# Kernel tuning notes

Hardware: AMD Instinct MI355X
Metric: run time of the kernel (lower is better)

Reference implementation:

```python
import jax, jax.numpy as jnp
import numpy as np

N_NODES = 50000
N_EDGES = 800000
N_PAIRS = 262144
F_IN, H1, H2, NCLS, HEADS = 572, 256, 128, 65, 2


def _bn(x, g, b, eps=1e-5):
    mu = x.mean(axis=0)
    var = x.var(axis=0)
    return g * (x - mu) * jax.lax.rsqrt(var + eps) + b


def _gat_conv(x, src, dst, W, a_src, a_dst, bias, heads, ch):
    """PyG GATConv, concat=False (mean over heads), negative_slope=0.2."""
    n = x.shape[0]
    h = (x @ W).reshape(n, heads, ch)                     # [N,H,C]
    s_n = (h * a_src[None]).sum(-1)                       # [N,H]
    d_n = (h * a_dst[None]).sum(-1)                       # [N,H]
    alpha = jax.nn.leaky_relu(s_n[src] + d_n[dst], 0.2)   # [E,H]
    m = jax.ops.segment_max(alpha, dst, num_segments=n)
    m = jnp.where(jnp.isfinite(m), m, 0.0)
    e = jnp.exp(alpha - m[dst])
    z = jax.ops.segment_sum(e, dst, num_segments=n)
    w = e / (z[dst] + 1e-16)                              # edge softmax per dst
    msg = h[src] * w[:, :, None]                          # [E,H,C]
    out = jax.ops.segment_sum(msg, dst, num_segments=n)   # [N,H,C]
    return out.mean(axis=1) + bias                        # concat=False -> mean


def setup_inputs() -> dict:
    key = jax.random.key(0)
    ks = jax.random.split(key, 24)
    g = lambda k, shp, fan: jax.random.normal(k, shp, jnp.float32) * (1.0 / np.sqrt(fan))
    inp = {
        "edge_index": jax.random.randint(ks[0], (2, N_EDGES), 0, N_NODES, jnp.int32),
        "x": jax.random.normal(ks[1], (N_NODES, F_IN), jnp.float32),
        "edge_id": jax.random.randint(ks[2], (2, N_PAIRS), 0, N_NODES, jnp.int32),
        "W1": g(ks[3], (F_IN, HEADS * H1), F_IN),
        "a_src1": g(ks[4], (HEADS, H1), H1),
        "a_dst1": g(ks[5], (HEADS, H1), H1),
        "b1": jnp.zeros((H1,), jnp.float32),
        "bn1_g": jnp.ones((H1,), jnp.float32), "bn1_b": jnp.zeros((H1,), jnp.float32),
        "W2": g(ks[6], (H1, HEADS * H1), H1),
        "a_src2": g(ks[7], (HEADS, H1), H1),
        "a_dst2": g(ks[8], (HEADS, H1), H1),
        "b2": jnp.zeros((H1,), jnp.float32),
        "bn2_g": jnp.ones((H1,), jnp.float32), "bn2_b": jnp.zeros((H1,), jnp.float32),
        "lw1": g(ks[9], (2 * H1, H2), 2 * H1), "lb1": jnp.zeros((H2,), jnp.float32),
        "bn3_g": jnp.ones((H2,), jnp.float32), "bn3_b": jnp.zeros((H2,), jnp.float32),
        "lw2": g(ks[10], (H2, H2), H2), "lb2": jnp.zeros((H2,), jnp.float32),
        "bn4_g": jnp.ones((H2,), jnp.float32), "bn4_b": jnp.zeros((H2,), jnp.float32),
        "fw": g(ks[11], (H2, NCLS), H2), "fb": jnp.zeros((NCLS,), jnp.float32),
    }
    return inp


def reference(edge_index, x, edge_id,
              W1, a_src1, a_dst1, b1, bn1_g, bn1_b,
              W2, a_src2, a_dst2, b2, bn2_g, bn2_b,
              lw1, lb1, bn3_g, bn3_b,
              lw2, lb2, bn4_g, bn4_b,
              fw, fb):
    n = x.shape[0]
    # PyG GATConv default add_self_loops=True
    loops = jnp.arange(n, dtype=edge_index.dtype)
    src = jnp.concatenate([edge_index[0], loops])
    dst = jnp.concatenate([edge_index[1], loops])

    h = _gat_conv(x, src, dst, W1, a_src1, a_dst1, b1, HEADS, H1)
    h = jax.nn.relu(_bn(h, bn1_g, bn1_b))
    h = _gat_conv(h, src, dst, W2, a_src2, a_dst2, b2, HEADS, H1)
    h = jax.nn.relu(_bn(h, bn2_g, bn2_b))

    pair = jnp.concatenate([h[edge_id[0]], h[edge_id[1]]], axis=1)  # [P, 2*H1]
    z = jax.nn.relu(_bn(pair @ lw1 + lb1, bn3_g, bn3_b))
    z = jax.nn.relu(_bn(z @ lw2 + lb2, bn4_g, bn4_b))
    return z @ fw + fb
```

## Files before the change

### kernel.cpp

```cpp
#include <hip/hip_runtime.h>

constexpr int NN = 50000;
constexpr int NE = 800000;
constexpr int NP = 262144;
constexpr int ET = NE + NN;

using short8 = __attribute__((ext_vector_type(8))) short;
using f32x4  = __attribute__((ext_vector_type(4))) float;

__device__ __forceinline__ ushort f2b(float f) {
  unsigned u = __float_as_uint(f);
  return (ushort)((u + 0x7FFFu + ((u >> 16) & 1u)) >> 16);
}
__device__ __forceinline__ float b2f(ushort b) {
  return __uint_as_float(((unsigned)b) << 16);
}

template<bool GATHER, bool OUT_BF16, bool STATS>
__global__ __launch_bounds__(256)
void mfma_gemm(const ushort* __restrict__ A, const ushort* __restrict__ BT,
               void* __restrict__ Cp, int M, int N, int Kpad, int Cld,
               const float* __restrict__ bias,
               const int* __restrict__ idx0, const int* __restrict__ idx1,
               double* __restrict__ stats)
{
  __shared__ __align__(16) ushort As[128 * 40];
  __shared__ __align__(16) ushort Bs[128 * 40];
  const int tid = threadIdx.x;
  const int lane = tid & 63;
  const int wave = tid >> 6;
  const int row0 = blockIdx.y * 128, col0 = blockIdx.x * 128;
  const int wm = (wave >> 1) * 64, wn = (wave & 1) * 64;
  const int lrow = lane & 15, lk = (lane >> 4) * 8;

  f32x4 acc[4][4];
  #pragma unroll
  for (int i = 0; i < 4; ++i)
    #pragma unroll
    for (int j = 0; j < 4; ++j)
      acc[i][j] = (f32x4){0.f, 0.f, 0.f, 0.f};

  for (int kt = 0; kt < Kpad; kt += 32) {
    #pragma unroll
    for (int c = tid; c < 512; c += 256) {
      int m = c >> 2, c8 = c & 3;
      int r = row0 + m;
      int kk = kt + c8 * 8;
      uint4 v = {0u, 0u, 0u, 0u};
      if (r < M) {
        const ushort* sp;
        if (GATHER) {
          int node = (kk < 256) ? idx0[r] : idx1[r];
          sp = A + (size_t)node * 256 + (kk & 255);
        } else {
          sp = A + (size_t)r * Kpad + kk;
        }
        v = *(const uint4*)sp;
      }
      *(uint4*)(As + m * 40 + c8 * 8) = v;
    }
    #pragma unroll
    for (int c = tid; c < 512; c += 256) {
      int n = c >> 2, c8 = c & 3;
      *(uint4*)(Bs + n * 40 + c8 * 8) =
          *(const uint4*)(BT + (size_t)(col0 + n) * Kpad + kt + c8 * 8);
    }
    __syncthreads();

    short8 af[4], bfr[4];
    #pragma unroll
    for (int i = 0; i < 4; ++i)
      af[i] = *(const short8*)(As + (wm + i * 16 + lrow) * 40 + lk);
    #pragma unroll
    for (int j = 0; j < 4; ++j)
      bfr[j] = *(const short8*)(Bs + (wn + j * 16 + lrow) * 40 + lk);
    #pragma unroll
    for (int i = 0; i < 4; ++i)
      #pragma unroll
      for (int j = 0; j < 4; ++j)
        acc[i][j] = __builtin_amdgcn_mfma_f32_16x16x32_bf16(af[i], bfr[j],
                                                            acc[i][j], 0, 0, 0);
    __syncthreads();
  }

  float* sacc = (float*)As;
  if constexpr (STATS) {
    sacc[tid] = 0.f;
    __syncthreads();
  }
  float cs[4] = {0.f, 0.f, 0.f, 0.f}, cq[4] = {0.f, 0.f, 0.f, 0.f};
  #pragma unroll
  for (int i = 0; i < 4; ++i) {
    int r0 = row0 + wm + i * 16 + (lane >> 4) * 4;
    #pragma unroll
    for (int j = 0; j < 4; ++j) {
      int col = col0 + wn + j * 16 + lrow;
      if (col >= N) continue;
      float bv = bias ? bias[col] : 0.f;
      #pragma unroll
      for (int rg = 0; rg < 4; ++rg) {
        int row = r0 + rg;
        if (row >= M) continue;
        float val = acc[i][j][rg] + bv;
        if (OUT_BF16)
          ((ushort*)Cp)[(size_t)row * Cld + col] = f2b(val);
        else
          ((float*)Cp)[(size_t)row * Cld + col] = val;
        if (STATS) { cs[j] += val; cq[j] += val * val; }
      }
    }
  }
  if constexpr (STATS) {
    #pragma unroll
    for (int j = 0; j < 4; ++j) {
      int cl = wn + j * 16 + lrow;
      atomicAdd(&sacc[2 * cl + 0], cs[j]);
      atomicAdd(&sacc[2 * cl + 1], cq[j]);
    }
    __syncthreads();
    if (tid < 128) {
      unsafeAtomicAdd(&stats[tid],       (double)sacc[2 * tid + 0]);
      unsafeAtomicAdd(&stats[128 + tid], (double)sacc[2 * tid + 1]);
    }
  }
}

__global__ void transpose_w(const float* __restrict__ W, ushort* __restrict__ BT,
                            int K, int N, int Kpad, int Npad)
{
  int i = blockIdx.x * blockDim.x + threadIdx.x;
  if (i >= Npad * Kpad) return;
  int n = i / Kpad, k = i % Kpad;
  float v = (n < N && k < K) ? W[(size_t)k * N + n] : 0.f;
  BT[i] = f2b(v);
}

__global__ void conv_x(const float* __restrict__ x, ushort* __restrict__ xb)
{
  int i = blockIdx.x * blockDim.x + threadIdx.x;
  if (i >= NN * 144) return;
  int r = i / 144, c4 = (i % 144) * 4;
  ushort4 o = {0, 0, 0, 0};
  if (c4 < 572) {
    float4 v = *(const float4*)(x + (size_t)r * 572 + c4);
    o.x = f2b(v.x); o.y = f2b(v.y); o.z = f2b(v.z); o.w = f2b(v.w);
  }
  *(ushort4*)(xb + (size_t)r * 576 + c4) = o;
}

__global__ void deg_count(const int* __restrict__ ei, int* __restrict__ deg)
{
  int e = blockIdx.x * blockDim.x + threadIdx.x;
  if (e >= ET) return;
  int dst = (e < NE) ? ei[NE + e] : e - NE;
  atomicAdd(&deg[dst], 1);
}

__global__ __launch_bounds__(1024)
void scan_deg(const int* __restrict__ deg, int* __restrict__ rowptr,
              int* __restrict__ cursor)
{
  __shared__ int tot[1024];
  const int t = threadIdx.x;
  const int CH = (NN + 1023) / 1024;
  const int base = t * CH;
  int s = 0;
  for (int i = 0; i < CH; ++i) {
    int idx = base + i;
    if (idx < NN) s += deg[idx];
  }
  tot[t] = s;
  __syncthreads();
  for (int off = 1; off < 1024; off <<= 1) {
    int v = (t >= off) ? tot[t - off] : 0;
    __syncthreads();
    tot[t] += v;
    __syncthreads();
  }
  int run = (t == 0) ? 0 : tot[t - 1];
  for (int i = 0; i < CH; ++i) {
    int idx = base + i;
    if (idx <= NN) { rowptr[idx] = run; if (idx < NN) cursor[idx] = run; }
    if (idx < NN) run += deg[idx];
  }
}

__global__ void scatter_edges(const int* __restrict__ ei, int* __restrict__ cursor,
                              int* __restrict__ csr_src)
{
  int e = blockIdx.x * blockDim.x + threadIdx.x;
  if (e >= ET) return;
  int src, dst;
  if (e < NE) { src = ei[e]; dst = ei[NE + e]; }
  else        { src = dst = e - NE; }
  int pos = atomicAdd(&cursor[dst], 1);
  csr_src[pos] = src;
}


__global__ void node_coeffs(const ushort* __restrict__ hb,
                            const float* __restrict__ a_src,
                            const float* __restrict__ a_dst,
                            float* __restrict__ s_n, float* __restrict__ d_n)
{
  int node = (blockIdx.x * blockDim.x + threadIdx.x) >> 6;
  int lane = threadIdx.x & 63;
  if (node >= NN) return;
  int head = lane >> 5;
  int cidx = (lane * 8) & 255;
  short8 hv = *(const short8*)(hb + (size_t)node * 512 + lane * 8);
  float4 a0 = *(const float4*)(a_src + head * 256 + cidx);
  float4 a1 = *(const float4*)(a_src + head * 256 + cidx + 4);
  float4 d0 = *(const float4*)(a_dst + head * 256 + cidx);
  float4 d1 = *(const float4*)(a_dst + head * 256 + cidx + 4);
  float h0 = b2f((ushort)hv[0]), h1 = b2f((ushort)hv[1]);
  float h2 = b2f((ushort)hv[2]), h3 = b2f((ushort)hv[3]);
  float h4 = b2f((ushort)hv[4]), h5 = b2f((ushort)hv[5]);
  float h6 = b2f((ushort)hv[6]), h7 = b2f((ushort)hv[7]);
  float ss = h0*a0.x + h1*a0.y + h2*a0.z + h3*a0.w
           + h4*a1.x + h5*a1.y + h6*a1.z + h7*a1.w;
  float dd = h0*d0.x + h1*d0.y + h2*d0.z + h3*d0.w
           + h4*d1.x + h5*d1.y + h6*d1.z + h7*d1.w;
  #pragma unroll
  for (int off = 16; off > 0; off >>= 1) {
    ss += __shfl_xor(ss, off);
    dd += __shfl_xor(dd, off);
  }
  if ((lane & 31) == 0) {
    s_n[node * 2 + head] = ss;
    d_n[node * 2 + head] = dd;
  }
}

__global__ __launch_bounds__(256)
void gat_aggregate(const int* __restrict__ rowptr, const int* __restrict__ csr_src,
                   const ushort* __restrict__ hb,
                   const float* __restrict__ s_n, const float* __restrict__ d_n,
                   const float* __restrict__ bias, float* __restrict__ outp,
                   double* __restrict__ stats)
{
  __shared__ float sacc[512];
  sacc[threadIdx.x] = 0.f;
  sacc[256 + threadIdx.x] = 0.f;
  __syncthreads();

  const int wave = threadIdx.x >> 6, lane = threadIdx.x & 63;
  const int base = blockIdx.x * 32 + wave * 8;
  const float4 bb = *(const float4*)(bias + lane * 4);
  const float2* sn2 = (const float2*)s_n;

  for (int n = 0; n < 8; ++n) {
    const int dst = base + n;
    if (dst < NN) {
      const int beg = rowptr[dst], end = rowptr[dst + 1];
      const float d0 = d_n[dst * 2 + 0], d1 = d_n[dst * 2 + 1];

      float m0 = -1e30f, m1 = -1e30f;
      for (int i = beg + lane; i < end; i += 64) {
        float2 sv = sn2[csr_src[i]];
        float a0 = sv.x + d0; a0 = a0 > 0.f ? a0 : 0.2f * a0;
        float a1 = sv.y + d1; a1 = a1 > 0.f ? a1 : 0.2f * a1;
        m0 = fmaxf(m0, a0); m1 = fmaxf(m1, a1);
      }
      #pragma unroll
      for (int off = 32; off > 0; off >>= 1) {
        m0 = fmaxf(m0, __shfl_xor(m0, off));
        m1 = fmaxf(m1, __shfl_xor(m1, off));
      }

      float z0 = 0.f, z1 = 0.f;
      for (int i = beg + lane; i < end; i += 64) {
        float2 sv = sn2[csr_src[i]];
        float a0 = sv.x + d0; a0 = a0 > 0.f ? a0 : 0.2f * a0;
        float a1 = sv.y + d1; a1 = a1 > 0.f ? a1 : 0.2f * a1;
        z0 += __expf(a0 - m0);
        z1 += __expf(a1 - m1);
      }
      #pragma unroll
      for (int off = 32; off > 0; off >>= 1) {
        z0 += __shfl_xor(z0, off);
        z1 += __shfl_xor(z1, off);
      }
      const float rz0 = 1.f / (z0 + 1e-16f);
      const float rz1 = 1.f / (z1 + 1e-16f);

      float4 acc0 = {0.f, 0.f, 0.f, 0.f};
      float4 acc1 = {0.f, 0.f, 0.f, 0.f};
      for (int i = beg; i < end; ++i) {
        int s = csr_src[i];
        float2 sv = sn2[s];
        float a0 = sv.x + d0; a0 = a0 > 0.f ? a0 : 0.2f * a0;
        float a1 = sv.y + d1; a1 = a1 > 0.f ? a1 : 0.2f * a1;
        float w0 = __expf(a0 - m0) * rz0;
        float w1 = __expf(a1 - m1) * rz1;
        ushort4 u0 = *(const ushort4*)(hb + (size_t)s * 512 + lane * 4);
        ushort4 u1 = *(const ushort4*)(hb + (size_t)s * 512 + 256 + lane * 4);
        acc0.x = fmaf(b2f(u0.x), w0, acc0.x); acc0.y = fmaf(b2f(u0.y), w0, acc0.y);
        acc0.z = fmaf(b2f(u0.z), w0, acc0.z); acc0.w = fmaf(b2f(u0.w), w0, acc0.w);
        acc1.x = fmaf(b2f(u1.x), w1, acc1.x); acc1.y = fmaf(b2f(u1.y), w1, acc1.y);
        acc1.z = fmaf(b2f(u1.z), w1, acc1.z); acc1.w = fmaf(b2f(u1.w), w1, acc1.w);
      }

      float4 o;
      o.x = 0.5f * (acc0.x + acc1.x) + bb.x;
      o.y = 0.5f * (acc0.y + acc1.y) + bb.y;
      o.z = 0.5f * (acc0.z + acc1.z) + bb.z;
      o.w = 0.5f * (acc0.w + acc1.w) + bb.w;
      *(float4*)(outp + (size_t)dst * 256 + lane * 4) = o;

      const int c = lane * 4;
      atomicAdd(&sacc[c + 0], o.x);       atomicAdd(&sacc[c + 1], o.y);
      atomicAdd(&sacc[c + 2], o.z);       atomicAdd(&sacc[c + 3], o.w);
      atomicAdd(&sacc[256 + c + 0], o.x * o.x);
      atomicAdd(&sacc[256 + c + 1], o.y * o.y);
      atomicAdd(&sacc[256 + c + 2], o.z * o.z);
      atomicAdd(&sacc[256 + c + 3], o.w * o.w);
    }
  }
  __syncthreads();
  const int c = threadIdx.x;
  unsafeAtomicAdd(&stats[c],       (double)sacc[c]);
  unsafeAtomicAdd(&stats[256 + c], (double)sacc[256 + c]);
}

__global__ void bn_prep(const double* __restrict__ stats,
                        const float* __restrict__ g, const float* __restrict__ b,
                        float* __restrict__ scale, float* __restrict__ shift,
                        int rows, int cols)
{
  int c = blockIdx.x * blockDim.x + threadIdx.x;
  if (c >= cols) return;
  float mean = (float)(stats[c] / rows);
  float var = (float)(stats[cols + c] / rows) - mean * mean;
  float rs = rsqrtf(var + 1e-5f);
  float sc = g[c] * rs;
  scale[c] = sc;
  shift[c] = b[c] - mean * sc;
}

__global__ void bn_apply_relu_b4(const float* __restrict__ x, ushort* __restrict__ y,
                                 const float* __restrict__ scale,
                                 const float* __restrict__ shift,
                                 int total4, int cols)
{
  int i = blockIdx.x * blockDim.x + threadIdx.x;
  if (i >= total4) return;
  int base = i * 4;
  int c = base % cols;
  float4 xv = *(const float4*)(x + base);
  float4 sv = *(const float4*)(scale + c);
  float4 tv = *(const float4*)(shift + c);
  ushort4 o;
  o.x = f2b(fmaxf(fmaf(xv.x, sv.x, tv.x), 0.f));
  o.y = f2b(fmaxf(fmaf(xv.y, sv.y, tv.y), 0.f));
  o.z = f2b(fmaxf(fmaf(xv.z, sv.z, tv.z), 0.f));
  o.w = f2b(fmaxf(fmaf(xv.w, sv.w, tv.w), 0.f));
  *(ushort4*)(y + base) = o;
}

static void gat_layer(const ushort* ain, int Kpad, const ushort* WT,
                      const float* asrc, const float* adst, const float* bias,
                      const float* bng, const float* bnb,
                      const int* rowptr, const int* csr_src,
                      ushort* hb, float* t, ushort* featb,
                      float* s_n, float* d_n, double* stats,
                      float* scale, float* shift, hipStream_t st)
{
  dim3 b256(256);
  mfma_gemm<false, true, false><<<dim3(4, 391), b256, 0, st>>>(
      ain, WT, hb, NN, 512, Kpad, 512, nullptr, nullptr, nullptr, nullptr);
  node_coeffs<<<(NN + 3) / 4, b256, 0, st>>>(hb, asrc, adst, s_n, d_n);
  gat_aggregate<<<(NN + 31) / 32, b256, 0, st>>>(rowptr, csr_src, hb,
                                                 s_n, d_n, bias, t, stats);
  bn_prep<<<1, 256, 0, st>>>(stats, bng, bnb, scale, shift, NN, 256);
  bn_apply_relu_b4<<<(NN * 64 + 255) / 256, b256, 0, st>>>(t, featb, scale, shift,
                                                           NN * 64, 256);
}

extern "C" void kernel_launch(void* const* d_in, const int* in_sizes, int n_in,
                              void* d_out, int out_size, void* d_ws, size_t ws_size,
                              hipStream_t stream)
{
  const int*   edge_index = (const int*)d_in[0];
  const float* x      = (const float*)d_in[1];
  const int*   edge_id = (const int*)d_in[2];
  const float* W1     = (const float*)d_in[3];
  const float* a_src1 = (const float*)d_in[4];
  const float* a_dst1 = (const float*)d_in[5];
  const float* b1     = (const float*)d_in[6];
  const float* bn1_g  = (const float*)d_in[7];
  const float* bn1_b  = (const float*)d_in[8];
  const float* W2     = (const float*)d_in[9];
  const float* a_src2 = (const float*)d_in[10];
  const float* a_dst2 = (const float*)d_in[11];
  const float* b2     = (const float*)d_in[12];
  const float* bn2_g  = (const float*)d_in[13];
  const float* bn2_b  = (const float*)d_in[14];
  const float* lw1    = (const float*)d_in[15];
  const float* lb1    = (const float*)d_in[16];
  const float* bn3_g  = (const float*)d_in[17];
  const float* bn3_b  = (const float*)d_in[18];
  const float* lw2    = (const float*)d_in[19];
  const float* lb2    = (const float*)d_in[20];
  const float* bn4_g  = (const float*)d_in[21];
  const float* bn4_b  = (const float*)d_in[22];
  const float* fw     = (const float*)d_in[23];
  const float* fb     = (const float*)d_in[24];
  float* out = (float*)d_out;

  char* w = (char*)d_ws;
  ushort* xb     = (ushort*)(w + 0);
  ushort* hb     = (ushort*)(w + 57600000);
  float*  t_buf  = (float*)(w + 108800000);
  ushort* feat1b = (ushort*)(w + 160000000);
  ushort* feat2b = (ushort*)(w + 185600000);
  float*  z1     = (float*)(w + 0);
  ushort* z1b    = (ushort*)(w + 160000000);
  float*  z2     = (float*)(w + 0);
  ushort* z2b    = (ushort*)(w + 227108864);
  int*    csr_src = (int*)(w + 294217728);
  int*    deg     = (int*)(w + 297700000);
  int*    rowptr  = (int*)(w + 297900000);
  int*    cursor  = (int*)(w + 298100008);
  float*  s_n     = (float*)(w + 298300008);
  float*  d_n     = (float*)(w + 298700008);
  double* stats   = (double*)(w + 299100008);
  float*  scaleb  = (float*)(w + 299200000);
  float*  shiftb  = (float*)(w + 299220000);
  ushort* W1T     = (ushort*)(w + 300000000);
  ushort* W2T     = (ushort*)(w + 300600000);
  ushort* LW1T    = (ushort*)(w + 300900000);
  ushort* LW2T    = (ushort*)(w + 301040000);
  ushort* FWT     = (ushort*)(w + 301080000);

  double* st1 = stats,        *st2 = stats + 512;
  double* st3 = stats + 1024, *st4 = stats + 1536;
  float* sc1 = scaleb, *sc2 = scaleb + 256, *sc3 = scaleb + 512, *sc4 = scaleb + 768;
  float* sh1 = shiftb, *sh2 = shiftb + 256, *sh3 = shiftb + 512, *sh4 = shiftb + 768;

  dim3 b256(256);

  hipMemsetAsync(stats, 0, 4 * 512 * sizeof(double), stream);

  transpose_w<<<(512 * 576 + 255) / 256, b256, 0, stream>>>(W1, W1T, 572, 512, 576, 512);
  transpose_w<<<(512 * 256 + 255) / 256, b256, 0, stream>>>(W2, W2T, 256, 512, 256, 512);
  transpose_w<<<(128 * 512 + 255) / 256, b256, 0, stream>>>(lw1, LW1T, 512, 128, 512, 128);
  transpose_w<<<(128 * 128 + 255) / 256, b256, 0, stream>>>(lw2, LW2T, 128, 128, 128, 128);
  transpose_w<<<(128 * 128 + 255) / 256, b256, 0, stream>>>(fw, FWT, 128, 65, 128, 128);
  conv_x<<<(NN * 144 + 255) / 256, b256, 0, stream>>>(x, xb);

  hipMemsetAsync(deg, 0, NN * sizeof(int), stream);
  deg_count<<<(ET + 255) / 256, b256, 0, stream>>>(edge_index, deg);
  scan_deg<<<1, 1024, 0, stream>>>(deg, rowptr, cursor);
  scatter_edges<<<(ET + 255) / 256, b256, 0, stream>>>(edge_index, cursor, csr_src);

  gat_layer(xb, 576, W1T, a_src1, a_dst1, b1, bn1_g, bn1_b, rowptr, csr_src,
            hb, t_buf, feat1b, s_n, d_n, st1, sc1, sh1, stream);
  gat_layer(feat1b, 256, W2T, a_src2, a_dst2, b2, bn2_g, bn2_b, rowptr, csr_src,
            hb, t_buf, feat2b, s_n, d_n, st2, sc2, sh2, stream);

  mfma_gemm<true, false, true><<<dim3(1, 2048), b256, 0, stream>>>(
      feat2b, LW1T, z1, NP, 128, 512, 128, lb1, edge_id, edge_id + NP, st3);
  bn_prep<<<1, 128, 0, stream>>>(st3, bn3_g, bn3_b, sc3, sh3, NP, 128);
  bn_apply_relu_b4<<<(NP * 32 + 255) / 256, b256, 0, stream>>>(z1, z1b, sc3, sh3,
                                                               NP * 32, 128);
  mfma_gemm<false, false, true><<<dim3(1, 2048), b256, 0, stream>>>(
      z1b, LW2T, z2, NP, 128, 128, 128, lb2, nullptr, nullptr, st4);
  bn_prep<<<1, 128, 0, stream>>>(st4, bn4_g, bn4_b, sc4, sh4, NP, 128);
  bn_apply_relu_b4<<<(NP * 32 + 255) / 256, b256, 0, stream>>>(z2, z2b, sc4, sh4,
                                                               NP * 32, 128);
  mfma_gemm<false, false, false><<<dim3(1, 2048), b256, 0, stream>>>(
      z2b, FWT, out, NP, 65, 128, 65, fb, nullptr, nullptr, nullptr);
}
```

Measured before the change: 1.488 ms.

## Fuse weight prep, fold BN prep into apply, unroll aggregate, cache gather indices

Merges the five weight transposes into one launch and drops the separate bn_prep kernels by computing scale and shift from the double stats inside the BN apply kernel. Gather indices for the pair GEMM are staged in shared memory instead of reloaded per K tile. The GAT aggregation handles 4 nodes per wave instead of 8 and unrolls the edge loop by two to keep more loads in flight. The trade-off is redundant per-element rsqrt and double math in BN apply, plus more blocks in the aggregation launch.

```diff
diff --git a/kernel.cpp b/kernel.cpp
--- a/kernel.cpp
+++ b/kernel.cpp
@@ -26,12 +26,22 @@
 {
   __shared__ __align__(16) ushort As[128 * 40];
   __shared__ __align__(16) ushort Bs[128 * 40];
+  __shared__ int idxs[256];
   const int tid = threadIdx.x;
   const int lane = tid & 63;
   const int wave = tid >> 6;
   const int row0 = blockIdx.y * 128, col0 = blockIdx.x * 128;
   const int wm = (wave >> 1) * 64, wn = (wave & 1) * 64;
   const int lrow = lane & 15, lk = (lane >> 4) * 8;
+
+  if constexpr (GATHER) {
+    if (tid < 128) {
+      int r = row0 + tid;
+      idxs[tid]       = (r < M) ? idx0[r] : 0;
+      idxs[128 + tid] = (r < M) ? idx1[r] : 0;
+    }
+    __syncthreads();
+  }
 
   f32x4 acc[4][4];
   #pragma unroll
@@ -50,7 +60,7 @@
       if (r < M) {
         const ushort* sp;
         if (GATHER) {
-          int node = (kk < 256) ? idx0[r] : idx1[r];
+          int node = (kk < 256) ? idxs[m] : idxs[128 + m];
           sp = A + (size_t)node * 256 + (kk & 255);
         } else {
           sp = A + (size_t)r * Kpad + kk;
@@ -125,11 +135,19 @@
   }
 }
 
-__global__ void transpose_w(const float* __restrict__ W, ushort* __restrict__ BT,
-                            int K, int N, int Kpad, int Npad)
+__global__ void prep_weights(const float* __restrict__ W1, ushort* __restrict__ W1T,
+                             const float* __restrict__ W2, ushort* __restrict__ W2T,
+                             const float* __restrict__ lw1, ushort* __restrict__ LW1T,
+                             const float* __restrict__ lw2, ushort* __restrict__ LW2T,
+                             const float* __restrict__ fw, ushort* __restrict__ FWT)
 {
   int i = blockIdx.x * blockDim.x + threadIdx.x;
-  if (i >= Npad * Kpad) return;
+  const float* W; ushort* BT; int K, N, Kpad;
+  if (i < 294912)      { W = W1;  BT = W1T;  K = 572; N = 512; Kpad = 576; }
+  else if (i < 425984) { i -= 294912; W = W2;  BT = W2T;  K = 256; N = 512; Kpad = 256; }
+  else if (i < 491520) { i -= 425984; W = lw1; BT = LW1T; K = 512; N = 128; Kpad = 512; }
+  else if (i < 507904) { i -= 491520; W = lw2; BT = LW2T; K = 128; N = 128; Kpad = 128; }
+  else                 { i -= 507904; W = fw;  BT = FWT;  K = 128; N = 65;  Kpad = 128; }
   int n = i / Kpad, k = i % Kpad;
   float v = (n < N && k < K) ? W[(size_t)k * N + n] : 0.f;
   BT[i] = f2b(v);
@@ -245,11 +263,11 @@
   __syncthreads();
 
   const int wave = threadIdx.x >> 6, lane = threadIdx.x & 63;
-  const int base = blockIdx.x * 32 + wave * 8;
+  const int base = blockIdx.x * 16 + wave * 4;
   const float4 bb = *(const float4*)(bias + lane * 4);
   const float2* sn2 = (const float2*)s_n;
 
-  for (int n = 0; n < 8; ++n) {
+  for (int n = 0; n < 4; ++n) {
     const int dst = base + n;
     if (dst < NN) {
       const int beg = rowptr[dst], end = rowptr[dst + 1];
@@ -286,7 +304,30 @@
 
       float4 acc0 = {0.f, 0.f, 0.f, 0.f};
       float4 acc1 = {0.f, 0.f, 0.f, 0.f};
-      for (int i = beg; i < end; ++i) {
+      int i = beg;
+      for (; i + 2 <= end; i += 2) {
+        int sA = csr_src[i], sB = csr_src[i + 1];
+        const ushort4 uA0 = *(const ushort4*)(hb + (size_t)sA * 512 + lane * 4);
+        const ushort4 uA1 = *(const ushort4*)(hb + (size_t)sA * 512 + 256 + lane * 4);
+        const ushort4 uB0 = *(const ushort4*)(hb + (size_t)sB * 512 + lane * 4);
+        const ushort4 uB1 = *(const ushort4*)(hb + (size_t)sB * 512 + 256 + lane * 4);
+        float2 svA = sn2[sA], svB = sn2[sB];
+        float aA0 = svA.x + d0; aA0 = aA0 > 0.f ? aA0 : 0.2f * aA0;
+        float aA1 = svA.y + d1; aA1 = aA1 > 0.f ? aA1 : 0.2f * aA1;
+        float aB0 = svB.x + d0; aB0 = aB0 > 0.f ? aB0 : 0.2f * aB0;
+        float aB1 = svB.y + d1; aB1 = aB1 > 0.f ? aB1 : 0.2f * aB1;
+        float wA0 = __expf(aA0 - m0) * rz0, wA1 = __expf(aA1 - m1) * rz1;
+        float wB0 = __expf(aB0 - m0) * rz0, wB1 = __expf(aB1 - m1) * rz1;
+        acc0.x = fmaf(b2f(uA0.x), wA0, acc0.x); acc0.y = fmaf(b2f(uA0.y), wA0, acc0.y);
+        acc0.z = fmaf(b2f(uA0.z), wA0, acc0.z); acc0.w = fmaf(b2f(uA0.w), wA0, acc0.w);
+        acc1.x = fmaf(b2f(uA1.x), wA1, acc1.x); acc1.y = fmaf(b2f(uA1.y), wA1, acc1.y);
+        acc1.z = fmaf(b2f(uA1.z), wA1, acc1.z); acc1.w = fmaf(b2f(uA1.w), wA1, acc1.w);
+        acc0.x = fmaf(b2f(uB0.x), wB0, acc0.x); acc0.y = fmaf(b2f(uB0.y), wB0, acc0.y);
+        acc0.z = fmaf(b2f(uB0.z), wB0, acc0.z); acc0.w = fmaf(b2f(uB0.w), wB0, acc0.w);
+        acc1.x = fmaf(b2f(uB1.x), wB1, acc1.x); acc1.y = fmaf(b2f(uB1.y), wB1, acc1.y);
+        acc1.z = fmaf(b2f(uB1.z), wB1, acc1.z); acc1.w = fmaf(b2f(uB1.w), wB1, acc1.w);
+      }
+      if (i < end) {
         int s = csr_src[i];
         float2 sv = sn2[s];
         float a0 = sv.x + d0; a0 = a0 > 0.f ? a0 : 0.2f * a0;
@@ -323,38 +364,28 @@
   unsafeAtomicAdd(&stats[256 + c], (double)sacc[256 + c]);
 }
 
-__global__ void bn_prep(const double* __restrict__ stats,
-                        const float* __restrict__ g, const float* __restrict__ b,
-                        float* __restrict__ scale, float* __restrict__ shift,
-                        int rows, int cols)
-{
-  int c = blockIdx.x * blockDim.x + threadIdx.x;
-  if (c >= cols) return;
-  float mean = (float)(stats[c] / rows);
-  float var = (float)(stats[cols + c] / rows) - mean * mean;
-  float rs = rsqrtf(var + 1e-5f);
-  float sc = g[c] * rs;
-  scale[c] = sc;
-  shift[c] = b[c] - mean * sc;
-}
-
 __global__ void bn_apply_relu_b4(const float* __restrict__ x, ushort* __restrict__ y,
-                                 const float* __restrict__ scale,
-                                 const float* __restrict__ shift,
-                                 int total4, int cols)
+                                 const double* __restrict__ stats,
+                                 const float* __restrict__ g, const float* __restrict__ b,
+                                 int total4, int cols, float inv_rows)
 {
   int i = blockIdx.x * blockDim.x + threadIdx.x;
   if (i >= total4) return;
   int base = i * 4;
   int c = base % cols;
   float4 xv = *(const float4*)(x + base);
-  float4 sv = *(const float4*)(scale + c);
-  float4 tv = *(const float4*)(shift + c);
+  float4 gv = *(const float4*)(g + c);
+  float4 bv = *(const float4*)(b + c);
   ushort4 o;
-  o.x = f2b(fmaxf(fmaf(xv.x, sv.x, tv.x), 0.f));
-  o.y = f2b(fmaxf(fmaf(xv.y, sv.y, tv.y), 0.f));
-  o.z = f2b(fmaxf(fmaf(xv.z, sv.z, tv.z), 0.f));
-  o.w = f2b(fmaxf(fmaf(xv.w, sv.w, tv.w), 0.f));
+  #pragma unroll
+  for (int k = 0; k < 4; ++k) {
+    float mean = (float)(stats[c + k] * (double)inv_rows);
+    float var = (float)(stats[cols + c + k] * (double)inv_rows) - mean * mean;
+    float sc = ((const float*)&gv)[k] * rsqrtf(var + 1e-5f);
+    float sh = ((const float*)&bv)[k] - mean * sc;
+    float v = fmaxf(fmaf(((const float*)&xv)[k], sc, sh), 0.f);
+    ((ushort*)&o)[k] = f2b(v);
+  }
   *(ushort4*)(y + base) = o;
 }
 
@@ -363,18 +394,16 @@
                       const float* bng, const float* bnb,
                       const int* rowptr, const int* csr_src,
                       ushort* hb, float* t, ushort* featb,
-                      float* s_n, float* d_n, double* stats,
-                      float* scale, float* shift, hipStream_t st)
+                      float* s_n, float* d_n, double* stats, hipStream_t st)
 {
   dim3 b256(256);
   mfma_gemm<false, true, false><<<dim3(4, 391), b256, 0, st>>>(
       ain, WT, hb, NN, 512, Kpad, 512, nullptr, nullptr, nullptr, nullptr);
   node_coeffs<<<(NN + 3) / 4, b256, 0, st>>>(hb, asrc, adst, s_n, d_n);
-  gat_aggregate<<<(NN + 31) / 32, b256, 0, st>>>(rowptr, csr_src, hb,
+  gat_aggregate<<<(NN + 15) / 16, b256, 0, st>>>(rowptr, csr_src, hb,
                                                  s_n, d_n, bias, t, stats);
-  bn_prep<<<1, 256, 0, st>>>(stats, bng, bnb, scale, shift, NN, 256);
-  bn_apply_relu_b4<<<(NN * 64 + 255) / 256, b256, 0, st>>>(t, featb, scale, shift,
-                                                           NN * 64, 256);
+  bn_apply_relu_b4<<<(NN * 64 + 255) / 256, b256, 0, st>>>(
+      t, featb, stats, bng, bnb, NN * 64, 256, 1.0f / NN);
 }
 
 extern "C" void kernel_launch(void* const* d_in, const int* in_sizes, int n_in,
@@ -425,8 +454,6 @@
   float*  s_n     = (float*)(w + 298300008);
   float*  d_n     = (float*)(w + 298700008);
   double* stats   = (double*)(w + 299100008);
-  float*  scaleb  = (float*)(w + 299200000);
-  float*  shiftb  = (float*)(w + 299220000);
   ushort* W1T     = (ushort*)(w + 300000000);
   ushort* W2T     = (ushort*)(w + 300600000);
   ushort* LW1T    = (ushort*)(w + 300900000);
@@ -435,18 +462,13 @@
 
   double* st1 = stats,        *st2 = stats + 512;
   double* st3 = stats + 1024, *st4 = stats + 1536;
-  float* sc1 = scaleb, *sc2 = scaleb + 256, *sc3 = scaleb + 512, *sc4 = scaleb + 768;
-  float* sh1 = shiftb, *sh2 = shiftb + 256, *sh3 = shiftb + 512, *sh4 = shiftb + 768;
 
   dim3 b256(256);
 
   hipMemsetAsync(stats, 0, 4 * 512 * sizeof(double), stream);
 
-  transpose_w<<<(512 * 576 + 255) / 256, b256, 0, stream>>>(W1, W1T, 572, 512, 576, 512);
-  transpose_w<<<(512 * 256 + 255) / 256, b256, 0, stream>>>(W2, W2T, 256, 512, 256, 512);
-  transpose_w<<<(128 * 512 + 255) / 256, b256, 0, stream>>>(lw1, LW1T, 512, 128, 512, 128);
-  transpose_w<<<(128 * 128 + 255) / 256, b256, 0, stream>>>(lw2, LW2T, 128, 128, 128, 128);
-  transpose_w<<<(128 * 128 + 255) / 256, b256, 0, stream>>>(fw, FWT, 128, 65, 128, 128);
+  prep_weights<<<2048, b256, 0, stream>>>(W1, W1T, W2, W2T, lw1, LW1T,
+                                          lw2, LW2T, fw, FWT);
   conv_x<<<(NN * 144 + 255) / 256, b256, 0, stream>>>(x, xb);
 
   hipMemsetAsync(deg, 0, NN * sizeof(int), stream);
@@ -455,20 +477,18 @@
   scatter_edges<<<(ET + 255) / 256, b256, 0, stream>>>(edge_index, cursor, csr_src);
 
   gat_layer(xb, 576, W1T, a_src1, a_dst1, b1, bn1_g, bn1_b, rowptr, csr_src,
-            hb, t_buf, feat1b, s_n, d_n, st1, sc1, sh1, stream);
+            hb, t_buf, feat1b, s_n, d_n, st1, stream);
   gat_layer(feat1b, 256, W2T, a_src2, a_dst2, b2, bn2_g, bn2_b, rowptr, csr_src,
-            hb, t_buf, feat2b, s_n, d_n, st2, sc2, sh2, stream);
+            hb, t_buf, feat2b, s_n, d_n, st2, stream);
 
   mfma_gemm<true, false, true><<<dim3(1, 2048), b256, 0, stream>>>(
       feat2b, LW1T, z1, NP, 128, 512, 128, lb1, edge_id, edge_id + NP, st3);
-  bn_prep<<<1, 128, 0, stream>>>(st3, bn3_g, bn3_b, sc3, sh3, NP, 128);
-  bn_apply_relu_b4<<<(NP * 32 + 255) / 256, b256, 0, stream>>>(z1, z1b, sc3, sh3,
-                                                               NP * 32, 128);
+  bn_apply_relu_b4<<<(NP * 32 + 255) / 256, b256, 0, stream>>>(
+      z1, z1b, st3, bn3_g, bn3_b, NP * 32, 128, 1.0f / NP);
   mfma_gemm<false, false, true><<<dim3(1, 2048), b256, 0, stream>>>(
       z1b, LW2T, z2, NP, 128, 128, 128, lb2, nullptr, nullptr, st4);
-  bn_prep<<<1, 128, 0, stream>>>(st4, bn4_g, bn4_b, sc4, sh4, NP, 128);
-  bn_apply_relu_b4<<<(NP * 32 + 255) / 256, b256, 0, stream>>>(z2, z2b, sc4, sh4,
-                                                               NP * 32, 128);
+  bn_apply_relu_b4<<<(NP * 32 + 255) / 256, b256, 0, stream>>>(
+      z2, z2b, st4, bn4_g, bn4_b, NP * 32, 128, 1.0f / NP);
   mfma_gemm<false, false, false><<<dim3(1, 2048), b256, 0, stream>>>(
       z2b, FWT, out, NP, 65, 128, 65, fb, nullptr, nullptr, nullptr);
 }
```

New measurement: 1.464 ms. No clear change (-1.6%).
